# Kernel tuning notes

Hardware: AMD Instinct MI355X
Metric: run time of the kernel (lower is better)

Reference implementation:

```python
import jax, jax.numpy as jnp
import numpy as np

B, DEC, F = 64, 12, 32        # batch, decoder steps, decoder feature size
L, H = 2, 512                 # gru layers, hidden size
E, T = 96, 4                  # encoder seq len, target size


def gru_cell(x, h, Wi, Wh, bi, bh):
    # PyTorch GRUCell math
    gi = x @ Wi.T + bi
    gh = h @ Wh.T + bh
    i_r, i_z, i_n = jnp.split(gi, 3, axis=-1)
    h_r, h_z, h_n = jnp.split(gh, 3, axis=-1)
    r = jax.nn.sigmoid(i_r + h_r)
    z = jax.nn.sigmoid(i_z + h_z)
    n = jnp.tanh(i_n + r * h_n)
    return (1.0 - z) * n + z * h


def setup_inputs() -> dict:
    key = jax.random.key(0)
    ks = jax.random.split(key, 12)
    s = lambda k, shape: jax.random.normal(k, shape, jnp.float32) * 0.02
    return {
        "inputs": jax.random.normal(ks[0], (B, DEC, F), jnp.float32),
        "hidden": jax.random.normal(ks[1], (L, B, H), jnp.float32) * 0.1,
        "enc_outputs": jax.random.normal(ks[2], (B, E, H), jnp.float32),
        "target_indices": jnp.arange(T, dtype=jnp.int32),
        "W_attn": s(ks[3], (H, 2 * H)),
        "b_attn": jnp.zeros((H,), jnp.float32),
        "v_attn": s(ks[4], (H,)),
        "gru_Wi0": s(ks[5], (3 * H, F + H)),
        "gru_Wh0": s(ks[6], (3 * H, H)),
        "gru_bi0": jnp.zeros((3 * H,), jnp.float32),
        "gru_bh0": jnp.zeros((3 * H,), jnp.float32),
        "gru_Wi1": s(ks[7], (3 * H, H)),
        "gru_Wh1": s(ks[8], (3 * H, H)),
        "gru_bi1": jnp.zeros((3 * H,), jnp.float32),
        "gru_bh1": jnp.zeros((3 * H,), jnp.float32),
        "W_out": s(ks[9], (T, 2 * H + F)),
        "b_out": jnp.zeros((T,), jnp.float32),
    }


def reference(inputs, hidden, enc_outputs, target_indices,
              W_attn, b_attn, v_attn,
              gru_Wi0, gru_Wh0, gru_bi0, gru_bh0,
              gru_Wi1, gru_Wh1, gru_bi1, gru_bh1,
              W_out, b_out):
    Hs = hidden.shape[-1]
    Wa_h, Wa_e = W_attn[:, :Hs], W_attn[:, Hs:]
    # encoder projection of the attn linear is constant over timesteps
    enc_proj = jnp.einsum('beh,gh->beg', enc_outputs, Wa_e)  # [B,E,H]
    layers = ((gru_Wi0, gru_Wh0, gru_bi0, gru_bh0),
              (gru_Wi1, gru_Wh1, gru_bi1, gru_bh1))

    def step(carry, x_t):
        h, cur = carry                     # h: [L,B,H], cur: [B,F]
        hl = h[-1]                         # final-layer hidden [B,H]
        energy = jnp.tanh(enc_proj + (hl @ Wa_h.T + b_attn)[:, None, :])
        w = jax.nn.softmax(energy @ v_attn, axis=1)          # [B,E]
        ws = jnp.einsum('be,beh->bh', w, enc_outputs)        # [B,H]
        x = jnp.concatenate([cur, ws], axis=-1)              # [B,F+H]
        new_h = []
        for l, (Wi, Wh, bi, bh) in enumerate(layers):
            hn = gru_cell(x, h[l], Wi, Wh, bi, bh)
            new_h.append(hn)
            x = hn
        out = jnp.concatenate([x, ws, cur], axis=-1) @ W_out.T + b_out  # [B,T]
        nxt = x_t.at[:, target_indices].set(out)  # feed prediction back
        return (jnp.stack(new_h), nxt), out

    xs = jnp.swapaxes(inputs, 0, 1)  # [DEC,B,F]
    (_, _), outs = jax.lax.scan(step, (hidden, inputs[:, 0, :]), xs)
    return jnp.swapaxes(outs, 0, 1)  # [B,DEC,T]
```

## Files before the change

### kernel.cpp

```cpp
#include <hip/hip_runtime.h>
#include <hip/hip_fp16.h>

#define NB   64
#define NDEC 12
#define NF   32
#define NH   512
#define NE   96
#define NT   4
#define KI0  (NF + NH)
#define KOUT (2*NH + NF)

typedef _Float16 half8_t __attribute__((ext_vector_type(8)));
typedef float   float4_t __attribute__((ext_vector_type(4)));

__device__ __forceinline__ float fast_tanh(float x) {
    x = fminf(fmaxf(x, -15.f), 15.f);
    float e = __expf(2.f * x);
    return (e - 1.f) / (e + 1.f);
}
__device__ __forceinline__ float fast_sig(float x) {
    return 1.f / (1.f + __expf(-x));
}

__global__ __launch_bounds__(256) void k_prep(
    const float* __restrict__ Wi0, const float* __restrict__ Wh0,
    const float* __restrict__ Wi1, const float* __restrict__ Wh1,
    const float* __restrict__ Wout, const float* __restrict__ Wattn,
    const float* __restrict__ hidden, const float* __restrict__ inputs,
    __half* __restrict__ Wi0h, __half* __restrict__ Wh0h,
    __half* __restrict__ Wi1h, __half* __restrict__ Wh1h,
    __half* __restrict__ Wouth, __half* __restrict__ WahH,
    __half* __restrict__ WaeH,
    float* __restrict__ h0row, float* __restrict__ h1row,
    __half* __restrict__ h0h, __half* __restrict__ h1h,
    __half* __restrict__ xcat_h)
{
    int i = blockIdx.x*256 + threadIdx.x;
    const int n0 = 1536*KI0, n1 = 1536*512, n4 = 4*KOUT, n5 = 512*512;
    if (i < n0) { Wi0h[i] = __float2half_rn(Wi0[i]); return; }  i -= n0;
    if (i < n1) { Wh0h[i] = __float2half_rn(Wh0[i]); return; }  i -= n1;
    if (i < n1) { Wi1h[i] = __float2half_rn(Wi1[i]); return; }  i -= n1;
    if (i < n1) { Wh1h[i] = __float2half_rn(Wh1[i]); return; }  i -= n1;
    if (i < n4) { Wouth[i] = __float2half_rn(Wout[i]); return; } i -= n4;
    if (i < n5) {
        int g = i >> 9, k = i & 511;
        WahH[i] = __float2half_rn(Wattn[(size_t)g*1024 + k]);
        return;
    }
    i -= n5;
    if (i < n5) {
        int g = i >> 9, k = i & 511;
        WaeH[i] = __float2half_rn(Wattn[(size_t)g*1024 + 512 + k]);
        return;
    }
    i -= n5;
    if (i < NB*NH) {
        int b = i >> 9, k = i & 511;
        float v0 = hidden[b*NH + k];
        float v1 = hidden[NB*NH + b*NH + k];
        h0row[b*NH + k] = v0;  h0h[b*NH + k] = __float2half_rn(v0);
        h1row[b*NH + k] = v1;  h1h[b*NH + k] = __float2half_rn(v1);
        return;
    }
    i -= NB*NH;
    if (i < NB*NF) {
        int b = i >> 5, k = i & 31;
        xcat_h[(size_t)b*KI0 + k] = __float2half_rn(inputs[b*NDEC*NF + k]);
    }
}

__global__ __launch_bounds__(256) void k_encproj(const float* __restrict__ enc,
                                                 const __half* __restrict__ WaeH,
                                                 __half* __restrict__ encph) {
    int x = blockIdx.x;
    int by = x >> 3, bx = x & 7;
    int t = threadIdx.x, w = t >> 6, lane = t & 63;
    int mr = lane & 15, kq = lane >> 4;
    int m = by*64 + w*16 + mr;
    const float* arow = enc + (size_t)m*NH;
    float4_t acc[4] = {{0.f,0.f,0.f,0.f},{0.f,0.f,0.f,0.f},
                       {0.f,0.f,0.f,0.f},{0.f,0.f,0.f,0.f}};
    for (int kb = 0; kb < NH; kb += 32) {
        int k = kb + kq*8;
        float4 a0 = *(const float4*)(arow + k);
        float4 a1 = *(const float4*)(arow + k + 4);
        half8_t a;
        a[0] = (_Float16)a0.x; a[1] = (_Float16)a0.y;
        a[2] = (_Float16)a0.z; a[3] = (_Float16)a0.w;
        a[4] = (_Float16)a1.x; a[5] = (_Float16)a1.y;
        a[6] = (_Float16)a1.z; a[7] = (_Float16)a1.w;
        #pragma unroll
        for (int j = 0; j < 4; ++j) {
            int n = bx*64 + j*16 + mr;
            half8_t b = *(const half8_t*)(WaeH + (size_t)n*NH + k);
            acc[j] = __builtin_amdgcn_mfma_f32_16x16x32_f16(a, b, acc[j], 0, 0, 0);
        }
    }
    #pragma unroll
    for (int j = 0; j < 4; ++j) {
        int col = bx*64 + j*16 + mr;
        #pragma unroll
        for (int r = 0; r < 4; ++r) {
            int row = by*64 + w*16 + kq*4 + r;
            encph[(size_t)row*NH + col] = __float2half_rn(acc[j][r]);
        }
    }
}

__global__ __launch_bounds__(256) void k_gemA(
    const float* __restrict__ inputs, const int* __restrict__ tgt,
    const __half* __restrict__ WahH, const float* __restrict__ battn,
    const __half* __restrict__ Wouth, const float* __restrict__ bout,
    const __half* __restrict__ Wh0h, const __half* __restrict__ Wh1h,
    const __half* __restrict__ h0h, const __half* __restrict__ h1h,
    __half* __restrict__ xcat_h,
    float* __restrict__ attc,
    float* __restrict__ ghb,
    float* __restrict__ out,
    int s, int att_on)
{
    int blk = blockIdx.x, t = threadIdx.x;
    int w = t >> 6, lane = t & 63;
    int mr = lane & 15, kq = lane >> 4;
    int gA = att_on ? 224 : 0;

    if (blk < gA) {
        int wid = blk*4 + w;
        if (wid < 128) {
            int rt = wid >> 2, bq = wid & 3;
            const __half* arow = WahH + (size_t)(rt*16 + mr)*NH;
            const __half* brow = h1h + (size_t)(bq*16 + mr)*NH;
            float4_t acc = {0.f,0.f,0.f,0.f};
            #pragma unroll 4
            for (int kb = 0; kb < NH; kb += 32) {
                half8_t a = *(const half8_t*)(arow + kb + kq*8);
                half8_t b = *(const half8_t*)(brow + kb + kq*8);
                acc = __builtin_amdgcn_mfma_f32_16x16x32_f16(a, b, acc, 0, 0, 0);
            }
            float* dst = attc + (size_t)(rt*16)*NB;
            #pragma unroll
            for (int r = 0; r < 4; ++r) {
                int grow = kq*4 + r;
                dst[(size_t)grow*NB + bq*16 + mr] = acc[r] + battn[rt*16 + grow];
            }
        } else {
            int gw = wid - 128;
            int rt = gw >> 2, bq = gw & 3;
            int layer = (rt >= 96) ? 1 : 0;
            int rloc = (rt - layer*96) * 16;
            const __half* Wh = layer ? Wh1h : Wh0h;
            const __half* Xh = layer ? h1h : h0h;
            const __half* arow = Wh + (size_t)(rloc + mr)*NH;
            const __half* brow = Xh + (size_t)(bq*16 + mr)*NH;
            float4_t acc = {0.f,0.f,0.f,0.f};
            #pragma unroll 4
            for (int kb = 0; kb < NH; kb += 32) {
                half8_t a = *(const half8_t*)(arow + kb + kq*8);
                half8_t b = *(const half8_t*)(brow + kb + kq*8);
                acc = __builtin_amdgcn_mfma_f32_16x16x32_f16(a, b, acc, 0, 0, 0);
            }
            float* gdst = ghb + ((size_t)layer*3*NH + rloc)*NB;
            #pragma unroll
            for (int r = 0; r < 4; ++r) {
                gdst[(size_t)(kq*4 + r)*NB + bq*16 + mr] = acc[r];
            }
        }
        return;
    }

    if (s == 0) return;
    int bq = w;
    int b = bq*16 + mr;
    const __half* h1b = h1h + (size_t)b*NH;
    const __half* xcb = xcat_h + (size_t)b*KI0;
    int ar = (mr < 4) ? mr : 3;
    const __half* arow = Wouth + (size_t)ar*KOUT;
    float4_t acc = {0.f,0.f,0.f,0.f};
    for (int kb = 0; kb < KOUT; kb += 32) {
        int k = kb + kq*8;
        half8_t a = *(const half8_t*)(arow + k);
        const __half* bp = (k < NH)   ? (h1b + k)
                         : (k < 2*NH) ? (xcb + NF + (k - NH))
                                      : (xcb + (k - 2*NH));
        half8_t bb = *(const half8_t*)bp;
        acc = __builtin_amdgcn_mfma_f32_16x16x32_f16(a, bb, acc, 0, 0, 0);
    }
    float o0 = __shfl(acc[0], mr) + bout[0];
    float o1 = __shfl(acc[1], mr) + bout[1];
    float o2 = __shfl(acc[2], mr) + bout[2];
    float o3 = __shfl(acc[3], mr) + bout[3];
    if (kq == 0) {
        *(float4*)(out + (size_t)b*(NDEC*NT) + (s-1)*NT) = make_float4(o0,o1,o2,o3);
    }
    if (s < NDEC) {
        int t0 = tgt[0], t1 = tgt[1], t2 = tgt[2], t3 = tgt[3];
        const float* ip = inputs + (size_t)b*(NDEC*NF) + (s-1)*NF;
        half8_t hv;
        #pragma unroll
        for (int i = 0; i < 8; ++i) {
            int f = kq*8 + i;
            float v = ip[f];
            v = (f == t0) ? o0 : (f == t1) ? o1 : (f == t2) ? o2 : (f == t3) ? o3 : v;
            hv[i] = (_Float16)__float2half_rn(v);
        }
        *(half8_t*)(xcat_h + (size_t)b*KI0 + kq*8) = hv;
    }
}

__global__ __launch_bounds__(1024) void k_soft(
    const float* __restrict__ vattn,
    const float* __restrict__ attc,
    const __half* __restrict__ encph, const float* __restrict__ enc,
    __half* __restrict__ xcat_h)
{
    int b = blockIdx.x, t = threadIdx.x;
    int lane = t & 63, widx = t >> 6;
    __shared__ float vs[NH], atts[NH];
    __shared__ float pes[NE], combA[NH], combB[NH];
    __shared__ float invD_sh;

    if (t < NH) { vs[t] = vattn[t]; atts[t] = attc[(size_t)t*NB + b]; }
    __syncthreads();

    {
        float ar[8], vr[8];
        #pragma unroll
        for (int i = 0; i < 8; ++i) { ar[i] = atts[lane*8 + i]; vr[i] = vs[lane*8 + i]; }
        for (int it = 0; it < 6; ++it) {
            int e = widx + it*16;
            const __half* ep = encph + ((size_t)(b*NE + e))*NH + lane*8;
            uint4 u = *(const uint4*)ep;
            __half2 p0 = *(__half2*)&u.x, p1 = *(__half2*)&u.y;
            __half2 p2 = *(__half2*)&u.z, p3 = *(__half2*)&u.w;
            float2 f0 = __half22float2(p0), f1 = __half22float2(p1);
            float2 f2 = __half22float2(p2), f3 = __half22float2(p3);
            float sacc;
            sacc  = fast_tanh(f0.x + ar[0]) * vr[0];
            sacc += fast_tanh(f0.y + ar[1]) * vr[1];
            sacc += fast_tanh(f1.x + ar[2]) * vr[2];
            sacc += fast_tanh(f1.y + ar[3]) * vr[3];
            sacc += fast_tanh(f2.x + ar[4]) * vr[4];
            sacc += fast_tanh(f2.y + ar[5]) * vr[5];
            sacc += fast_tanh(f3.x + ar[6]) * vr[6];
            sacc += fast_tanh(f3.y + ar[7]) * vr[7];
            #pragma unroll
            for (int off = 32; off; off >>= 1) sacc += __shfl_down(sacc, off);
            if (lane == 0) pes[e] = __expf(sacc);
        }
    }
    __syncthreads();

    if (t < 64) {
        float v = pes[t] + ((t < 32) ? pes[64 + t] : 0.f);
        #pragma unroll
        for (int off = 32; off; off >>= 1) v += __shfl_down(v, off);
        if (t == 0) invD_sh = 1.f / v;
    }
    __syncthreads();

    {
        int k = t & 511, half = t >> 9;
        const float* eb = enc + ((size_t)b*NE + half*48)*NH + k;
        float acc = 0.f;
        #pragma unroll 4
        for (int e = 0; e < 48; ++e) acc += pes[half*48 + e] * eb[(size_t)e*NH];
        if (half == 0) combA[k] = acc; else combB[k] = acc;
    }
    __syncthreads();
    if (t < NH) {
        float v = (combA[t] + combB[t]) * invD_sh;
        xcat_h[(size_t)b*KI0 + NF + t] = __float2half_rn(v);
    }
}

__global__ __launch_bounds__(256) void k_gru(
    const __half* __restrict__ Wi,
    const float* __restrict__ bi, const float* __restrict__ bh,
    const __half* __restrict__ xh, int K,
    const float* __restrict__ ghbL,
    const float* __restrict__ hold,
    float* __restrict__ hnew,
    __half* __restrict__ hnewh)
{
    int blk = blockIdx.x, t = threadIdx.x;
    int w = t >> 6, lane = t & 63;
    int mr = lane & 15, kq = lane >> 4;
    int jg = blk >> 2, bq = blk & 3;
    int j0 = jg*16, b0 = bq*16;
    __shared__ float gis[3][16][17];

    if (w < 3) {
        int gate = w;
        const __half* arow = Wi + (size_t)(gate*NH + j0 + mr)*K;
        const __half* brow = xh + (size_t)(b0 + mr)*K;
        float4_t acc = {0.f,0.f,0.f,0.f};
        #pragma unroll 4
        for (int kb = 0; kb < K; kb += 32) {
            half8_t a = *(const half8_t*)(arow + kb + kq*8);
            half8_t b = *(const half8_t*)(brow + kb + kq*8);
            acc = __builtin_amdgcn_mfma_f32_16x16x32_f16(a, b, acc, 0, 0, 0);
        }
        #pragma unroll
        for (int r = 0; r < 4; ++r) gis[gate][kq*4 + r][mr] = acc[r];
    }
    __syncthreads();

    int jl = t >> 4, bl = t & 15;
    int j = j0 + jl, b = b0 + bl;
    float S0 = gis[0][jl][bl], S1 = gis[1][jl][bl], S2 = gis[2][jl][bl];
    float ghr = ghbL[(size_t)(0*NH + j)*NB + b];
    float ghz = ghbL[(size_t)(1*NH + j)*NB + b];
    float ghn = ghbL[(size_t)(2*NH + j)*NB + b];
    float r = fast_sig(S0 + ghr + bi[j] + bh[j]);
    float z = fast_sig(S1 + ghz + bi[NH + j] + bh[NH + j]);
    float n = fast_tanh(S2 + bi[2*NH + j] + r*(ghn + bh[2*NH + j]));
    float hp = hold[(size_t)b*NH + j];
    float hv = (1.f - z)*n + z*hp;
    hnew[(size_t)b*NH + j] = hv;
    hnewh[(size_t)b*NH + j] = __float2half_rn(hv);
}

extern "C" void kernel_launch(void* const* d_in, const int* in_sizes, int n_in,
                              void* d_out, int out_size, void* d_ws, size_t ws_size,
                              hipStream_t stream) {
    const float* inputs = (const float*)d_in[0];
    const float* hidden = (const float*)d_in[1];
    const float* enc    = (const float*)d_in[2];
    const int*   tgt    = (const int*)d_in[3];
    const float* Wattn  = (const float*)d_in[4];
    const float* battn  = (const float*)d_in[5];
    const float* vattn  = (const float*)d_in[6];
    const float* Wi0    = (const float*)d_in[7];
    const float* Wh0    = (const float*)d_in[8];
    const float* bi0    = (const float*)d_in[9];
    const float* bh0    = (const float*)d_in[10];
    const float* Wi1    = (const float*)d_in[11];
    const float* Wh1    = (const float*)d_in[12];
    const float* bi1    = (const float*)d_in[13];
    const float* bh1    = (const float*)d_in[14];
    const float* Wout   = (const float*)d_in[15];
    const float* bout   = (const float*)d_in[16];
    float* out = (float*)d_out;

    float* h0row  = (float*)d_ws;
    float* h1row  = h0row + NB*NH;
    float* ghb    = h1row + NB*NH;
    float* attc   = ghb + 2*3*NH*NB;
    __half* Wi0h  = (__half*)(attc + NH*NB);
    __half* Wh0h  = Wi0h + 1536*KI0;
    __half* Wi1h  = Wh0h + 1536*NH;
    __half* Wh1h  = Wi1h + 1536*NH;
    __half* Wouth = Wh1h + 1536*NH;
    __half* WahH  = Wouth + 4*KOUT;
    __half* WaeH  = WahH + NH*NH;
    __half* h0h   = WaeH + NH*NH;
    __half* h1h   = h0h + NB*NH;
    __half* xcat_h= h1h + NB*NH;
    __half* encph = xcat_h + NB*KI0;

    const int prep_n = 1536*KI0 + 3*1536*NH + 4*KOUT + 2*NH*NH + NB*NH + NB*NF;
    k_prep<<<(prep_n + 255)/256, 256, 0, stream>>>(
        Wi0, Wh0, Wi1, Wh1, Wout, Wattn, hidden, inputs,
        Wi0h, Wh0h, Wi1h, Wh1h, Wouth, WahH, WaeH,
        h0row, h1row, h0h, h1h, xcat_h);
    k_encproj<<<768, 256, 0, stream>>>(enc, WaeH, encph);

    for (int s = 0; s < NDEC; ++s) {
        k_gemA<<<(s == 0) ? 224 : 225, 256, 0, stream>>>(
            inputs, tgt, WahH, battn, Wouth, bout, Wh0h, Wh1h,
            h0h, h1h, xcat_h, attc, ghb, out, s, 1);
        k_soft<<<NB, 1024, 0, stream>>>(vattn, attc, encph, enc, xcat_h);
        k_gru<<<128, 256, 0, stream>>>(Wi0h, bi0, bh0,
                                       xcat_h, KI0,
                                       ghb,
                                       h0row, h0row, h0h);
        k_gru<<<128, 256, 0, stream>>>(Wi1h, bi1, bh1,
                                       h0h, NH,
                                       ghb + 3*NH*NB,
                                       h1row, h1row, h1h);
    }
    k_gemA<<<1, 256, 0, stream>>>(
        inputs, tgt, WahH, battn, Wouth, bout, Wh0h, Wh1h,
        h0h, h1h, xcat_h, attc, ghb, out, NDEC, 0);
}
```

Before: 596.7 us.

## Split-K the GEMV tiles across waves in gemA and gru kernels

```diff
diff --git a/kernel.cpp b/kernel.cpp
--- a/kernel.cpp
+++ b/kernel.cpp
@@ -122,49 +122,50 @@
     int blk = blockIdx.x, t = threadIdx.x;
     int w = t >> 6, lane = t & 63;
     int mr = lane & 15, kq = lane >> 4;
-    int gA = att_on ? 224 : 0;
+    int gA = att_on ? 896 : 0;
+    __shared__ float parts[4][16][17];
 
     if (blk < gA) {
-        int wid = blk*4 + w;
-        if (wid < 128) {
-            int rt = wid >> 2, bq = wid & 3;
-            const __half* arow = WahH + (size_t)(rt*16 + mr)*NH;
-            const __half* brow = h1h + (size_t)(bq*16 + mr)*NH;
-            float4_t acc = {0.f,0.f,0.f,0.f};
-            #pragma unroll 4
-            for (int kb = 0; kb < NH; kb += 32) {
-                half8_t a = *(const half8_t*)(arow + kb + kq*8);
-                half8_t b = *(const half8_t*)(brow + kb + kq*8);
-                acc = __builtin_amdgcn_mfma_f32_16x16x32_f16(a, b, acc, 0, 0, 0);
-            }
-            float* dst = attc + (size_t)(rt*16)*NB;
-            #pragma unroll
-            for (int r = 0; r < 4; ++r) {
-                int grow = kq*4 + r;
-                dst[(size_t)grow*NB + bq*16 + mr] = acc[r] + battn[rt*16 + grow];
-            }
+        const __half* arow;
+        const __half* brow;
+        float* dst;
+        int is_att, rt16;
+        if (blk < 128) {
+            int rt = blk >> 2, bq = blk & 3;
+            rt16 = rt*16;
+            arow = WahH + (size_t)(rt16 + mr)*NH;
+            brow = h1h + (size_t)(bq*16 + mr)*NH;
+            dst  = attc + (size_t)rt16*NB + bq*16;
+            is_att = 1;
         } else {
-            int gw = wid - 128;
+            int gw = blk - 128;
             int rt = gw >> 2, bq = gw & 3;
             int layer = (rt >= 96) ? 1 : 0;
             int rloc = (rt - layer*96) * 16;
+            rt16 = rloc;
             const __half* Wh = layer ? Wh1h : Wh0h;
             const __half* Xh = layer ? h1h : h0h;
-            const __half* arow = Wh + (size_t)(rloc + mr)*NH;
-            const __half* brow = Xh + (size_t)(bq*16 + mr)*NH;
-            float4_t acc = {0.f,0.f,0.f,0.f};
-            #pragma unroll 4
-            for (int kb = 0; kb < NH; kb += 32) {
-                half8_t a = *(const half8_t*)(arow + kb + kq*8);
-                half8_t b = *(const half8_t*)(brow + kb + kq*8);
-                acc = __builtin_amdgcn_mfma_f32_16x16x32_f16(a, b, acc, 0, 0, 0);
-            }
-            float* gdst = ghb + ((size_t)layer*3*NH + rloc)*NB;
-            #pragma unroll
-            for (int r = 0; r < 4; ++r) {
-                gdst[(size_t)(kq*4 + r)*NB + bq*16 + mr] = acc[r];
-            }
-        }
+            arow = Wh + (size_t)(rloc + mr)*NH;
+            brow = Xh + (size_t)(bq*16 + mr)*NH;
+            dst  = ghb + ((size_t)layer*3*NH + rloc)*NB + bq*16;
+            is_att = 0;
+        }
+        int kb0 = w*128;
+        float4_t acc = {0.f,0.f,0.f,0.f};
+        #pragma unroll
+        for (int kb = kb0; kb < kb0 + 128; kb += 32) {
+            half8_t a = *(const half8_t*)(arow + kb + kq*8);
+            half8_t b = *(const half8_t*)(brow + kb + kq*8);
+            acc = __builtin_amdgcn_mfma_f32_16x16x32_f16(a, b, acc, 0, 0, 0);
+        }
+        #pragma unroll
+        for (int r = 0; r < 4; ++r) parts[w][kq*4 + r][mr] = acc[r];
+        __syncthreads();
+        int jl = t >> 4, bl = t & 15;
+        float v = parts[0][jl][bl] + parts[1][jl][bl]
+                + parts[2][jl][bl] + parts[3][jl][bl];
+        if (is_att) v += battn[rt16 + jl];
+        dst[(size_t)jl*NB + bl] = v;
         return;
     }
 
@@ -273,7 +274,7 @@
     }
 }
 
-__global__ __launch_bounds__(256) void k_gru(
+__global__ __launch_bounds__(768) void k_gru(
     const __half* __restrict__ Wi,
     const float* __restrict__ bi, const float* __restrict__ bh,
     const __half* __restrict__ xh, int K,
@@ -287,37 +288,46 @@
     int mr = lane & 15, kq = lane >> 4;
     int jg = blk >> 2, bq = blk & 3;
     int j0 = jg*16, b0 = bq*16;
-    __shared__ float gis[3][16][17];
-
-    if (w < 3) {
-        int gate = w;
-        const __half* arow = Wi + (size_t)(gate*NH + j0 + mr)*K;
-        const __half* brow = xh + (size_t)(b0 + mr)*K;
-        float4_t acc = {0.f,0.f,0.f,0.f};
-        #pragma unroll 4
-        for (int kb = 0; kb < K; kb += 32) {
-            half8_t a = *(const half8_t*)(arow + kb + kq*8);
-            half8_t b = *(const half8_t*)(brow + kb + kq*8);
-            acc = __builtin_amdgcn_mfma_f32_16x16x32_f16(a, b, acc, 0, 0, 0);
-        }
-        #pragma unroll
-        for (int r = 0; r < 4; ++r) gis[gate][kq*4 + r][mr] = acc[r];
-    }
-    __syncthreads();
-
-    int jl = t >> 4, bl = t & 15;
-    int j = j0 + jl, b = b0 + bl;
-    float S0 = gis[0][jl][bl], S1 = gis[1][jl][bl], S2 = gis[2][jl][bl];
-    float ghr = ghbL[(size_t)(0*NH + j)*NB + b];
-    float ghz = ghbL[(size_t)(1*NH + j)*NB + b];
-    float ghn = ghbL[(size_t)(2*NH + j)*NB + b];
-    float r = fast_sig(S0 + ghr + bi[j] + bh[j]);
-    float z = fast_sig(S1 + ghz + bi[NH + j] + bh[NH + j]);
-    float n = fast_tanh(S2 + bi[2*NH + j] + r*(ghn + bh[2*NH + j]));
-    float hp = hold[(size_t)b*NH + j];
-    float hv = (1.f - z)*n + z*hp;
-    hnew[(size_t)b*NH + j] = hv;
-    hnewh[(size_t)b*NH + j] = __float2half_rn(hv);
+    __shared__ float parts[3][4][16][17];
+
+    int gate = w >> 2, c = w & 3;
+    int nsteps = K >> 5;
+    int rem = nsteps & 3;
+    int base = c*(nsteps >> 2) + ((c < rem) ? c : rem);
+    int cnt  = (nsteps >> 2) + ((c < rem) ? 1 : 0);
+    const __half* arow = Wi + (size_t)(gate*NH + j0 + mr)*K;
+    const __half* brow = xh + (size_t)(b0 + mr)*K;
+    float4_t acc = {0.f,0.f,0.f,0.f};
+    for (int i2 = 0; i2 < cnt; ++i2) {
+        int kb = (base + i2)*32;
+        half8_t a = *(const half8_t*)(arow + kb + kq*8);
+        half8_t b = *(const half8_t*)(brow + kb + kq*8);
+        acc = __builtin_amdgcn_mfma_f32_16x16x32_f16(a, b, acc, 0, 0, 0);
+    }
+    #pragma unroll
+    for (int r = 0; r < 4; ++r) parts[gate][c][kq*4 + r][mr] = acc[r];
+    __syncthreads();
+
+    if (t < 256) {
+        int jl = t >> 4, bl = t & 15;
+        int j = j0 + jl, b = b0 + bl;
+        float S0 = parts[0][0][jl][bl] + parts[0][1][jl][bl]
+                 + parts[0][2][jl][bl] + parts[0][3][jl][bl];
+        float S1 = parts[1][0][jl][bl] + parts[1][1][jl][bl]
+                 + parts[1][2][jl][bl] + parts[1][3][jl][bl];
+        float S2 = parts[2][0][jl][bl] + parts[2][1][jl][bl]
+                 + parts[2][2][jl][bl] + parts[2][3][jl][bl];
+        float ghr = ghbL[(size_t)(0*NH + j)*NB + b];
+        float ghz = ghbL[(size_t)(1*NH + j)*NB + b];
+        float ghn = ghbL[(size_t)(2*NH + j)*NB + b];
+        float r = fast_sig(S0 + ghr + bi[j] + bh[j]);
+        float z = fast_sig(S1 + ghz + bi[NH + j] + bh[NH + j]);
+        float n = fast_tanh(S2 + bi[2*NH + j] + r*(ghn + bh[2*NH + j]));
+        float hp = hold[(size_t)b*NH + j];
+        float hv = (1.f - z)*n + z*hp;
+        hnew[(size_t)b*NH + j] = hv;
+        hnewh[(size_t)b*NH + j] = __float2half_rn(hv);
+    }
 }
 
 extern "C" void kernel_launch(void* const* d_in, const int* in_sizes, int n_in,
@@ -366,15 +376,15 @@
     k_encproj<<<768, 256, 0, stream>>>(enc, WaeH, encph);
 
     for (int s = 0; s < NDEC; ++s) {
-        k_gemA<<<(s == 0) ? 224 : 225, 256, 0, stream>>>(
+        k_gemA<<<(s == 0) ? 896 : 897, 256, 0, stream>>>(
             inputs, tgt, WahH, battn, Wouth, bout, Wh0h, Wh1h,
             h0h, h1h, xcat_h, attc, ghb, out, s, 1);
         k_soft<<<NB, 1024, 0, stream>>>(vattn, attc, encph, enc, xcat_h);
-        k_gru<<<128, 256, 0, stream>>>(Wi0h, bi0, bh0,
+        k_gru<<<128, 768, 0, stream>>>(Wi0h, bi0, bh0,
                                        xcat_h, KI0,
                                        ghb,
                                        h0row, h0row, h0h);
-        k_gru<<<128, 256, 0, stream>>>(Wi1h, bi1, bh1,
+        k_gru<<<128, 768, 0, stream>>>(Wi1h, bi1, bh1,
                                        h0h, NH,
                                        ghb + 3*NH*NB,
                                        h1row, h1row, h1h);
```

Measured after the change: 576.6 us. 3.4% less time.
